# Optimization experiments

Hardware: AMD Instinct MI355X
Metric: run time of the kernel (lower is better)

## Reference

```python
import jax, jax.numpy as jnp
import numpy as np

BATCH = 16384
INPUT_DIM = 1024
OUTPUT_DIM = 256
SCALES = 5  # pywt level = SCALES - 1

# pywt db4 decomposition low-pass filter (ascending index order)
DB4_LO = jnp.array([
    -0.010597401785069032, 0.0328830116668852, 0.030841381835560764,
    -0.18703481171909309, -0.027983769416859854, 0.6308807679298589,
    0.7148465705529157, 0.2303778133088965], dtype=jnp.float32)
# QMF: dec_hi[k] = (-1)^(k+1) * dec_lo[L-1-k]  (matches pywt sign convention)
_SIGNS = jnp.array([-1.0, 1.0, -1.0, 1.0, -1.0, 1.0, -1.0, 1.0], dtype=jnp.float32)
DB4_HI = DB4_LO[::-1] * _SIGNS


def _dwt_step(x, lo, hi):
    """Single-level pywt dwt with 'symmetric' mode along the last axis.
    x: [B, N] -> (cA, cD) each [B, floor((N+L-1)/2)]."""
    L = lo.shape[0]
    left = x[:, L - 2::-1]          # symmetric (half-point) left extension, L-1 samples
    right = x[:, -1:-L:-1]          # symmetric right extension, L-1 samples
    e = jnp.concatenate([left, x, right], axis=-1)[:, 1:]  # drop 1 to align odd-index downsample
    # convolution == correlation with reversed filter; stride-2 valid conv
    kern = jnp.stack([lo[::-1], hi[::-1]])[:, None, :]      # [2, 1, L]
    y = jax.lax.conv_general_dilated(
        e[:, None, :], kern, window_strides=(2,), padding='VALID',
        dimension_numbers=('NCW', 'OIW', 'NCW'))            # [B, 2, out_len]
    return y[:, 0], y[:, 1]


def _wavedec(x, level):
    """pywt.wavedec(x, 'db4', level) -> [cA_level, cD_level, ..., cD_1]."""
    ca = x
    details = []
    for _ in range(level):
        ca, cd = _dwt_step(ca, DB4_LO, DB4_HI)
        details.append(cd)
    return [ca] + details[::-1]


def setup_inputs() -> dict:
    key = jax.random.key(0)
    ks = jax.random.split(key, SCALES + 1)
    inp = {"x": jax.random.normal(ks[0], (BATCH, INPUT_DIM), dtype=jnp.float32)}
    for s in range(SCALES):
        inp[f"basis{s}"] = jax.random.normal(
            ks[s + 1], (INPUT_DIM // 2 ** s, OUTPUT_DIM), dtype=jnp.float32)
    return inp


def reference(x, basis0, basis1, basis2, basis3, basis4):
    bases = [basis0, basis1, basis2, basis3, basis4]
    coeffs = _wavedec(x, SCALES - 1)  # [cA4, cD4, cD3, cD2, cD1]
    out = jnp.zeros((x.shape[0], OUTPUT_DIM), dtype=x.dtype)
    for s in range(SCALES):
        m = min(coeffs[s].shape[-1], bases[s].shape[0])  # static; truncate to common length
        out = out + coeffs[s][:, :m] @ bases[s][:m]
    return out
```

## Files before the change

### kernel.cpp

```cpp
#include <hip/hip_runtime.h>
#include <stdint.h>

#define BATCH   16384
#define INDIM   1024
#define OUTDIM  256

constexpr int KP = 480;

typedef __attribute__((ext_vector_type(8))) short short8;
typedef __attribute__((ext_vector_type(4))) float f32x4;

__device__ __constant__ float LORc[8] = { 0.2303778133088965f,   0.7148465705529157f,
                                          0.6308807679298589f,  -0.027983769416859854f,
                                         -0.18703481171909309f,  0.030841381835560764f,
                                          0.0328830116668852f,  -0.010597401785069032f };
__device__ __constant__ float HIRc[8] = {-0.010597401785069032f, -0.0328830116668852f,
                                          0.030841381835560764f,  0.18703481171909309f,
                                         -0.027983769416859854f, -0.6308807679298589f,
                                          0.7148465705529157f,   -0.2303778133088965f };

__device__ __forceinline__ float symx(const float* __restrict__ in, int N, int t) {
    if (t < 0)  t = -1 - t;
    if (t >= N) t = 2 * N - 1 - t;
    return in[t];
}

__device__ __forceinline__ void dwt_level(const float* __restrict__ in, int N, int M,
                                          float* __restrict__ outA,
                                          float* __restrict__ outD, int nD, int lane) {
    for (int i = lane; i < M; i += 64) {
        const int base = 2 * i - 6;
        float a = 0.f, d = 0.f;
        if (base >= 0 && base + 7 < N) {
            #pragma unroll
            for (int k = 0; k < 8; ++k) {
                const float v = in[base + k];
                a = fmaf(v, LORc[k], a);
                d = fmaf(v, HIRc[k], d);
            }
        } else {
            #pragma unroll
            for (int k = 0; k < 8; ++k) {
                const float v = symx(in, N, base + k);
                a = fmaf(v, LORc[k], a);
                d = fmaf(v, HIRc[k], d);
            }
        }
        outA[i] = a;
        if (i < nD) outD[i] = d;
    }
}

__device__ __forceinline__ ushort f2bf_rne(float f) {
    union { float f; uint32_t u; } v; v.f = f;
    uint32_t r = v.u + 0x7fffu + ((v.u >> 16) & 1u);
    return (ushort)(r >> 16);
}
__device__ __forceinline__ float bf2f(ushort h) {
    union { uint32_t u; float f; } v; v.u = ((uint32_t)h) << 16;
    return v.f;
}

__device__ __forceinline__ void split2(float a0, float a1, uint32_t& hw, uint32_t& lw) {
    const uint32_t u0 = __float_as_uint(a0), u1 = __float_as_uint(a1);
    const uint32_t r0 = u0 + 0x7fffu + ((u0 >> 16) & 1u);
    const uint32_t r1 = u1 + 0x7fffu + ((u1 >> 16) & 1u);
    hw = (r0 >> 16) | (r1 & 0xffff0000u);
    const float l0 = a0 - __uint_as_float(r0 & 0xffff0000u);
    const float l1 = a1 - __uint_as_float(r1 & 0xffff0000u);
    const uint32_t v0 = __float_as_uint(l0), v1 = __float_as_uint(l1);
    const uint32_t s0 = v0 + 0x7fffu + ((v0 >> 16) & 1u);
    const uint32_t s1 = v1 + 0x7fffu + ((v1 >> 16) & 1u);
    lw = (s0 >> 16) | (s1 & 0xffff0000u);
}

extern "C" __global__ __launch_bounds__(256)
void prep1(const float* __restrict__ b0, const float* __restrict__ b1,
           const float* __restrict__ b2, const float* __restrict__ b3,
           const float* __restrict__ b4,
           float* __restrict__ Wc, float* __restrict__ Bp)
{
    __shared__ float buf[4][1544];
    const int tid = threadIdx.x;
    if (blockIdx.x < 256) {
        const int wid  = tid >> 6;
        const int lane = tid & 63;
        const int row  = blockIdx.x * 4 + wid;
        float* bufA = buf[wid];
        float* bufB = bufA + 1024;
        float* crow = Wc + (size_t)row * KP;
        for (int j = lane; j < 1024; j += 64) bufA[j] = (j == row) ? 1.f : 0.f;
        __syncthreads();
        dwt_level(bufA, 1024, 515, bufB, crow + 408, 64, lane);
        __syncthreads();
        dwt_level(bufB, 515, 261, bufA, crow + 280, 128, lane);
        __syncthreads();
        dwt_level(bufA, 261, 134, bufB, crow + 144, 134, lane);
        __syncthreads();
        dwt_level(bufB, 134, 70, crow, crow + 72, 70, lane);
        if (lane < 14) {
            const int padidx[14] = {70,71,142,143,278,279,472,473,474,475,476,477,478,479};
            crow[padidx[lane]] = 0.f;
        }
    } else {
        const int k  = (blockIdx.x - 256) * 4 + (tid >> 6);
        const int n0 = (tid & 63) * 4;
        float4 v = float4{0.f, 0.f, 0.f, 0.f};
        if      (k < 70)              v = *(const float4*)(b0 + (size_t)k * OUTDIM + n0);
        else if (k >= 72  && k < 142) v = *(const float4*)(b1 + (size_t)(k - 72)  * OUTDIM + n0);
        else if (k >= 144 && k < 278) v = *(const float4*)(b2 + (size_t)(k - 144) * OUTDIM + n0);
        else if (k >= 280 && k < 408) v = *(const float4*)(b3 + (size_t)(k - 280) * OUTDIM + n0);
        else if (k >= 408 && k < 472) v = *(const float4*)(b4 + (size_t)(k - 408) * OUTDIM + n0);
        *(float4*)(Bp + (size_t)k * OUTDIM + n0) = v;
    }
}

extern "C" __global__ __launch_bounds__(256)
void prep2(const float* __restrict__ Wc, const float* __restrict__ Bp,
           ushort* __restrict__ Bpk)
{
    __shared__ float wc[8][KP];
    const int tid = threadIdx.x;
    const int k0  = blockIdx.x * 8;
    const int r   = tid >> 5;
    for (int k = (tid & 31); k < KP; k += 32)
        wc[r][k] = Wc[(size_t)(k0 + r) * KP + k];
    __syncthreads();

    float acc[8] = {0,0,0,0,0,0,0,0};
    for (int k = 0; k < KP; ++k) {
        const float b = Bp[(size_t)k * OUTDIM + tid];
        #pragma unroll
        for (int j = 0; j < 8; ++j) acc[j] = fmaf(wc[j][k], b, acc[j]);
    }

    const int chunk = blockIdx.x >> 2, kg = blockIdx.x & 3;
    const int nf = tid >> 4, ln = tid & 15;
    const int lane = kg * 16 + ln;
    ushort h[8], l[8];
    #pragma unroll
    for (int j = 0; j < 8; ++j) {
        h[j] = f2bf_rne(acc[j]);
        l[j] = f2bf_rne(acc[j] - bf2f(h[j]));
    }
    const size_t base = ((size_t)(chunk * 16 + nf) * 2) * 512 + (size_t)lane * 8;
    uint4 hv = { (uint32_t)h[0] | ((uint32_t)h[1] << 16), (uint32_t)h[2] | ((uint32_t)h[3] << 16),
                 (uint32_t)h[4] | ((uint32_t)h[5] << 16), (uint32_t)h[6] | ((uint32_t)h[7] << 16) };
    uint4 lv = { (uint32_t)l[0] | ((uint32_t)l[1] << 16), (uint32_t)l[2] | ((uint32_t)l[3] << 16),
                 (uint32_t)l[4] | ((uint32_t)l[5] << 16), (uint32_t)l[6] | ((uint32_t)l[7] << 16) };
    *(uint4*)(Bpk + base)       = hv;
    *(uint4*)(Bpk + base + 512) = lv;
}

extern "C" __global__ __launch_bounds__(512, 4)
void wkan_mfma(const float* __restrict__ x, const ushort* __restrict__ Bpk,
               float* __restrict__ out)
{
    __shared__ ushort Bb[2][8][2][64][8];
    __shared__ ushort Ah[2][2][2][2][64][8];

    const int tid  = threadIdx.x;
    const int lane = tid & 63;
    const int wid  = tid >> 6;
    const int wm   = wid >> 2;
    const int wn   = wid & 3;
    const int row0 = blockIdx.x * 64;
    const int nf0  = blockIdx.y * 8;

    const int srow  = tid >> 3;
    const int sk0   = (tid & 7) << 2;
    const int slane = (sk0 >> 3) * 16 + (srow & 15);
    const int sj0   = sk0 & 7;
    const int swm   = srow >> 5, smf = (srow >> 4) & 1;

    const float*  agp = x + (size_t)(row0 + srow) * INDIM + sk0;
    const ushort* bgp = Bpk + (size_t)nf0 * 1024 + (size_t)tid * 8;

    f32x4 acc[2][2];
    #pragma unroll
    for (int m = 0; m < 2; ++m)
        #pragma unroll
        for (int f = 0; f < 2; ++f) acc[m][f] = f32x4{0.f, 0.f, 0.f, 0.f};

    float4 av; uint4 bv0, bv1;

    av  = *(const float4*)(agp);
    bv0 = *(const uint4*)(bgp);
    bv1 = *(const uint4*)(bgp + 4096);
    {
        uint32_t hw0, lw0, hw1, lw1;
        split2(av.x, av.y, hw0, lw0);
        split2(av.z, av.w, hw1, lw1);
        *(uint2*)&Ah[0][swm][smf][0][slane][sj0] = uint2{hw0, hw1};
        *(uint2*)&Ah[0][swm][smf][1][slane][sj0] = uint2{lw0, lw1};
        ushort* bd = &Bb[0][0][0][0][0] + (size_t)tid * 8;
        *(uint4*)bd          = bv0;
        *(uint4*)(bd + 4096) = bv1;
    }
    av  = *(const float4*)(agp + 32);
    bv0 = *(const uint4*)(bgp + 16384);
    bv1 = *(const uint4*)(bgp + 16384 + 4096);
    __syncthreads();

    for (int c = 0; c < 32; ++c) {
        const int cur = c & 1, nx = cur ^ 1;

        if (c < 31) {
            uint32_t hw0, lw0, hw1, lw1;
            split2(av.x, av.y, hw0, lw0);
            split2(av.z, av.w, hw1, lw1);
            *(uint2*)&Ah[nx][swm][smf][0][slane][sj0] = uint2{hw0, hw1};
            *(uint2*)&Ah[nx][swm][smf][1][slane][sj0] = uint2{lw0, lw1};
            ushort* bd = &Bb[nx][0][0][0][0] + (size_t)tid * 8;
            *(uint4*)bd          = bv0;
            *(uint4*)(bd + 4096) = bv1;
        }
        if (c < 30) {
            av = *(const float4*)(agp + (size_t)(c + 2) * 32);
            const ushort* bs = bgp + (size_t)(c + 2) * 16384;
            bv0 = *(const uint4*)bs;
            bv1 = *(const uint4*)(bs + 4096);
        }

        short8 afr[2][2], bfr[2][2];
        #pragma unroll
        for (int m = 0; m < 2; ++m)
            #pragma unroll
            for (int h = 0; h < 2; ++h)
                afr[m][h] = *(const short8*)&Ah[cur][wm][m][h][lane][0];
        #pragma unroll
        for (int f = 0; f < 2; ++f)
            #pragma unroll
            for (int h = 0; h < 2; ++h)
                bfr[f][h] = *(const short8*)&Bb[cur][wn * 2 + f][h][lane][0];

        #pragma unroll
        for (int m = 0; m < 2; ++m)
            #pragma unroll
            for (int f = 0; f < 2; ++f) {
                acc[m][f] = __builtin_amdgcn_mfma_f32_16x16x32_bf16(afr[m][0], bfr[f][0], acc[m][f], 0, 0, 0);
                acc[m][f] = __builtin_amdgcn_mfma_f32_16x16x32_bf16(afr[m][0], bfr[f][1], acc[m][f], 0, 0, 0);
                acc[m][f] = __builtin_amdgcn_mfma_f32_16x16x32_bf16(afr[m][1], bfr[f][0], acc[m][f], 0, 0, 0);
            }
        __syncthreads();
    }

    #pragma unroll
    for (int m = 0; m < 2; ++m)
        #pragma unroll
        for (int f = 0; f < 2; ++f) {
            const int col  = nf0 * 16 + wn * 32 + f * 16 + (lane & 15);
            const int rowb = row0 + wm * 32 + m * 16 + (lane >> 4) * 4;
            #pragma unroll
            for (int r = 0; r < 4; ++r)
                out[(size_t)(rowb + r) * OUTDIM + col] = acc[m][f][r];
        }
}

constexpr int F_ROWS = 32;
constexpr int F_KP   = 472;

__device__ __forceinline__ void dwt_level_f(const float* __restrict__ in, int N, int M,
                                            float* __restrict__ outA,
                                            float* __restrict__ outD, int nD, int ht) {
    for (int i = ht; i < M; i += 128) {
        const int base = 2 * i - 6;
        float a = 0.f, d = 0.f;
        #pragma unroll
        for (int k = 0; k < 8; ++k) {
            const float v = symx(in, N, base + k);
            a = fmaf(v, LORc[k], a);
            d = fmaf(v, HIRc[k], d);
        }
        outA[i] = a;
        if (i < nD) outD[i] = d;
    }
}

extern "C" __global__ __launch_bounds__(256, 2)
void wkan_fused(const float* __restrict__ x,
                const float* __restrict__ b0, const float* __restrict__ b1,
                const float* __restrict__ b2, const float* __restrict__ b3,
                const float* __restrict__ b4,
                float* __restrict__ out)
{
    extern __shared__ float smem[];
    float* coef = smem;
    float* wbuf = smem + F_ROWS * F_KP;

    const int tid  = threadIdx.x;
    const int row0 = blockIdx.x * F_ROWS;

    for (int i = tid; i < F_ROWS * F_KP / 4; i += 256)
        ((float4*)coef)[i] = float4{0.f, 0.f, 0.f, 0.f};
    __syncthreads();

    const int slot = tid >> 7;
    const int ht   = tid & 127;
    float* bufA = wbuf + slot * 1544;
    float* bufB = bufA + 1024;

    for (int it = 0; it < F_ROWS / 2; ++it) {
        const int r = it * 2 + slot;
        float* crow = coef + r * F_KP;
        const float* xrow = x + (size_t)(row0 + r) * INDIM;
        ((float4*)bufA)[ht]       = ((const float4*)xrow)[ht];
        ((float4*)bufA)[ht + 128] = ((const float4*)xrow)[ht + 128];
        __syncthreads();
        dwt_level_f(bufA, 1024, 515, bufB, crow + 408, 64, ht);
        __syncthreads();
        dwt_level_f(bufB, 515, 261, bufA, crow + 280, 128, ht);
        __syncthreads();
        dwt_level_f(bufA, 261, 134, bufB, crow + 144, 134, ht);
        __syncthreads();
        dwt_level_f(bufB, 134, 70, crow, crow + 72, 70, ht);
        __syncthreads();
    }

    const int rg = tid >> 5;
    const int cg = tid & 31;
    float acc[4][8];
    #pragma unroll
    for (int r = 0; r < 4; ++r)
        #pragma unroll
        for (int c = 0; c < 8; ++c) acc[r][c] = 0.f;

    const float* Bs[5]  = { b0, b1, b2, b3, b4 };
    const int    off[5] = { 0, 72, 144, 280, 408 };
    const int    l4[5]  = { 72, 72, 136, 128, 64 };

    for (int s = 0; s < 5; ++s) {
        const float* __restrict__ B = Bs[s];
        const int o = off[s], L = l4[s];
        for (int k = 0; k < L; k += 4) {
            float4 bb[4][2];
            #pragma unroll
            for (int kk = 0; kk < 4; ++kk) {
                const float* bp = B + (size_t)(k + kk) * OUTDIM + cg * 8;
                bb[kk][0] = *(const float4*)(bp);
                bb[kk][1] = *(const float4*)(bp + 4);
            }
            #pragma unroll
            for (int rr = 0; rr < 4; ++rr) {
                const float4 c4 = *(const float4*)(coef + (rg * 4 + rr) * F_KP + o + k);
                const float cv[4] = { c4.x, c4.y, c4.z, c4.w };
                #pragma unroll
                for (int kk = 0; kk < 4; ++kk) {
                    acc[rr][0] = fmaf(cv[kk], bb[kk][0].x, acc[rr][0]);
                    acc[rr][1] = fmaf(cv[kk], bb[kk][0].y, acc[rr][1]);
                    acc[rr][2] = fmaf(cv[kk], bb[kk][0].z, acc[rr][2]);
                    acc[rr][3] = fmaf(cv[kk], bb[kk][0].w, acc[rr][3]);
                    acc[rr][4] = fmaf(cv[kk], bb[kk][1].x, acc[rr][4]);
                    acc[rr][5] = fmaf(cv[kk], bb[kk][1].y, acc[rr][5]);
                    acc[rr][6] = fmaf(cv[kk], bb[kk][1].z, acc[rr][6]);
                    acc[rr][7] = fmaf(cv[kk], bb[kk][1].w, acc[rr][7]);
                }
            }
        }
    }

    #pragma unroll
    for (int rr = 0; rr < 4; ++rr) {
        float* op = out + (size_t)(row0 + rg * 4 + rr) * OUTDIM + cg * 8;
        *(float4*)(op)     = float4{ acc[rr][0], acc[rr][1], acc[rr][2], acc[rr][3] };
        *(float4*)(op + 4) = float4{ acc[rr][4], acc[rr][5], acc[rr][6], acc[rr][7] };
    }
}

extern "C" void kernel_launch(void* const* d_in, const int* in_sizes, int n_in,
                              void* d_out, int out_size, void* d_ws, size_t ws_size,
                              hipStream_t stream) {
    const float* x  = (const float*)d_in[0];
    const float* b0 = (const float*)d_in[1];
    const float* b1 = (const float*)d_in[2];
    const float* b2 = (const float*)d_in[3];
    const float* b3 = (const float*)d_in[4];
    const float* b4 = (const float*)d_in[5];
    float* out = (float*)d_out;

    const size_t nWc  = (size_t)1024 * KP;
    const size_t nBp  = (size_t)KP * OUTDIM;
    const size_t nBpk = (size_t)1024 * OUTDIM * 2;
    const size_t need = (nWc + nBp) * 4 + nBpk * 2;

    if (ws_size >= need) {
        float*  Wc  = (float*)d_ws;
        float*  Bp  = Wc + nWc;
        ushort* Bpk = (ushort*)(Bp + nBp);

        hipLaunchKernelGGL(prep1, dim3(376), dim3(256), 0, stream,
                           b0, b1, b2, b3, b4, Wc, Bp);
        hipLaunchKernelGGL(prep2, dim3(128), dim3(256), 0, stream, Wc, Bp, Bpk);
        hipLaunchKernelGGL(wkan_mfma, dim3(BATCH / 64, 2), dim3(512), 0, stream,
                           x, Bpk, out);
    } else {
        const size_t shmem = (size_t)(F_ROWS * F_KP + 2 * 1544) * sizeof(float);
        hipLaunchKernelGGL(wkan_fused, dim3(BATCH / F_ROWS), dim3(256), shmem, stream,
                           x, b0, b1, b2, b3, b4, out);
    }
}
```

Measured before the change: 160.9 us.

## Widen MFMA tile to full output width and deepen x prefetch

The main GEMM kernel now has each block compute all 256 output columns instead of splitting N across two blocks. This removes the duplicate loading and bf16 splitting of x rows, at the cost of twice the B staging per block and dynamic LDS of 80KB. The x loads are prefetched four chunks ahead through a small register ring. The A hi part now uses truncation instead of round-to-nearest before the residual split. __syncthreads is replaced by an explicit lgkmcnt wait plus s_barrier, and the occupancy hint in launch bounds is dropped.

```diff
diff --git a/kernel.cpp b/kernel.cpp
--- a/kernel.cpp
+++ b/kernel.cpp
@@ -61,13 +61,11 @@
     return v.f;
 }
 
-__device__ __forceinline__ void split2(float a0, float a1, uint32_t& hw, uint32_t& lw) {
+__device__ __forceinline__ void splitc(float a0, float a1, uint32_t& hw, uint32_t& lw) {
     const uint32_t u0 = __float_as_uint(a0), u1 = __float_as_uint(a1);
-    const uint32_t r0 = u0 + 0x7fffu + ((u0 >> 16) & 1u);
-    const uint32_t r1 = u1 + 0x7fffu + ((u1 >> 16) & 1u);
-    hw = (r0 >> 16) | (r1 & 0xffff0000u);
-    const float l0 = a0 - __uint_as_float(r0 & 0xffff0000u);
-    const float l1 = a1 - __uint_as_float(r1 & 0xffff0000u);
+    hw = (u0 >> 16) | (u1 & 0xffff0000u);
+    const float l0 = a0 - __uint_as_float(u0 & 0xffff0000u);
+    const float l1 = a1 - __uint_as_float(u1 & 0xffff0000u);
     const uint32_t v0 = __float_as_uint(l0), v1 = __float_as_uint(l1);
     const uint32_t s0 = v0 + 0x7fffu + ((v0 >> 16) & 1u);
     const uint32_t s1 = v1 + 0x7fffu + ((v1 >> 16) & 1u);
@@ -152,12 +150,13 @@
     *(uint4*)(Bpk + base + 512) = lv;
 }
 
-extern "C" __global__ __launch_bounds__(512, 4)
+extern "C" __global__ __launch_bounds__(512)
 void wkan_mfma(const float* __restrict__ x, const ushort* __restrict__ Bpk,
                float* __restrict__ out)
 {
-    __shared__ ushort Bb[2][8][2][64][8];
-    __shared__ ushort Ah[2][2][2][2][64][8];
+    extern __shared__ __align__(16) ushort sm[];
+    ushort* Bb0 = sm;
+    ushort* Ah0 = sm + 32768;
 
     const int tid  = threadIdx.x;
     const int lane = tid & 63;
@@ -165,91 +164,113 @@
     const int wm   = wid >> 2;
     const int wn   = wid & 3;
     const int row0 = blockIdx.x * 64;
-    const int nf0  = blockIdx.y * 8;
-
-    const int srow  = tid >> 3;
-    const int sk0   = (tid & 7) << 2;
-    const int slane = (sk0 >> 3) * 16 + (srow & 15);
-    const int sj0   = sk0 & 7;
-    const int swm   = srow >> 5, smf = (srow >> 4) & 1;
-
+
+    const int srow = tid >> 3;
+    const int sk0  = (tid & 7) << 2;
+    const int smf  = srow >> 4;
+    const int slan = ((sk0 >> 3) << 4) | (srow & 15);
+    const int sj0  = sk0 & 7;
+    const int awoff = ((smf * 2 + 0) * 64 + slan) * 8 + sj0;
     const float*  agp = x + (size_t)(row0 + srow) * INDIM + sk0;
-    const ushort* bgp = Bpk + (size_t)nf0 * 1024 + (size_t)tid * 8;
-
-    f32x4 acc[2][2];
+    const ushort* bgp = Bpk + (size_t)tid * 8;
+
+    f32x4 acc[2][4];
     #pragma unroll
     for (int m = 0; m < 2; ++m)
         #pragma unroll
-        for (int f = 0; f < 2; ++f) acc[m][f] = f32x4{0.f, 0.f, 0.f, 0.f};
-
-    float4 av; uint4 bv0, bv1;
-
-    av  = *(const float4*)(agp);
+        for (int f = 0; f < 4; ++f) acc[m][f] = f32x4{0.f, 0.f, 0.f, 0.f};
+
+    float4 av[4];
+    uint4  bv0, bv1, bv2, bv3;
+
+    av[0] = *(const float4*)agp;
     bv0 = *(const uint4*)(bgp);
     bv1 = *(const uint4*)(bgp + 4096);
+    bv2 = *(const uint4*)(bgp + 8192);
+    bv3 = *(const uint4*)(bgp + 12288);
+    av[1] = *(const float4*)(agp + 32);
+    av[2] = *(const float4*)(agp + 64);
+    av[3] = *(const float4*)(agp + 96);
     {
         uint32_t hw0, lw0, hw1, lw1;
-        split2(av.x, av.y, hw0, lw0);
-        split2(av.z, av.w, hw1, lw1);
-        *(uint2*)&Ah[0][swm][smf][0][slane][sj0] = uint2{hw0, hw1};
-        *(uint2*)&Ah[0][swm][smf][1][slane][sj0] = uint2{lw0, lw1};
-        ushort* bd = &Bb[0][0][0][0][0] + (size_t)tid * 8;
-        *(uint4*)bd          = bv0;
-        *(uint4*)(bd + 4096) = bv1;
-    }
-    av  = *(const float4*)(agp + 32);
-    bv0 = *(const uint4*)(bgp + 16384);
-    bv1 = *(const uint4*)(bgp + 16384 + 4096);
-    __syncthreads();
-
+        splitc(av[0].x, av[0].y, hw0, lw0);
+        splitc(av[0].z, av[0].w, hw1, lw1);
+        *(uint2*)(Ah0 + awoff)       = uint2{hw0, hw1};
+        *(uint2*)(Ah0 + awoff + 512) = uint2{lw0, lw1};
+        ushort* bd = Bb0 + tid * 8;
+        *(uint4*)(bd)         = bv0;
+        *(uint4*)(bd + 4096)  = bv1;
+        *(uint4*)(bd + 8192)  = bv2;
+        *(uint4*)(bd + 12288) = bv3;
+    }
+    {
+        const ushort* bs = bgp + 16384;
+        bv0 = *(const uint4*)(bs);
+        bv1 = *(const uint4*)(bs + 4096);
+        bv2 = *(const uint4*)(bs + 8192);
+        bv3 = *(const uint4*)(bs + 12288);
+    }
+    asm volatile("s_waitcnt lgkmcnt(0)\n\ts_barrier" ::: "memory");
+
+    #pragma unroll 4
     for (int c = 0; c < 32; ++c) {
-        const int cur = c & 1, nx = cur ^ 1;
+        const int cur = c & 1;
+        ushort* Bbc = Bb0 + cur * 16384;
+        ushort* Ahc = Ah0 + cur * 4096;
+        ushort* Bbn = Bb0 + (cur ^ 1) * 16384;
+        ushort* Ahn = Ah0 + (cur ^ 1) * 4096;
 
         if (c < 31) {
+            const float4 a = av[(c + 1) & 3];
             uint32_t hw0, lw0, hw1, lw1;
-            split2(av.x, av.y, hw0, lw0);
-            split2(av.z, av.w, hw1, lw1);
-            *(uint2*)&Ah[nx][swm][smf][0][slane][sj0] = uint2{hw0, hw1};
-            *(uint2*)&Ah[nx][swm][smf][1][slane][sj0] = uint2{lw0, lw1};
-            ushort* bd = &Bb[nx][0][0][0][0] + (size_t)tid * 8;
-            *(uint4*)bd          = bv0;
-            *(uint4*)(bd + 4096) = bv1;
+            splitc(a.x, a.y, hw0, lw0);
+            splitc(a.z, a.w, hw1, lw1);
+            *(uint2*)(Ahn + awoff)       = uint2{hw0, hw1};
+            *(uint2*)(Ahn + awoff + 512) = uint2{lw0, lw1};
+            ushort* bd = Bbn + tid * 8;
+            *(uint4*)(bd)         = bv0;
+            *(uint4*)(bd + 4096)  = bv1;
+            *(uint4*)(bd + 8192)  = bv2;
+            *(uint4*)(bd + 12288) = bv3;
         }
         if (c < 30) {
-            av = *(const float4*)(agp + (size_t)(c + 2) * 32);
             const ushort* bs = bgp + (size_t)(c + 2) * 16384;
-            bv0 = *(const uint4*)bs;
+            bv0 = *(const uint4*)(bs);
             bv1 = *(const uint4*)(bs + 4096);
-        }
-
-        short8 afr[2][2], bfr[2][2];
+            bv2 = *(const uint4*)(bs + 8192);
+            bv3 = *(const uint4*)(bs + 12288);
+        }
+        if (c < 28) av[c & 3] = *(const float4*)(agp + (size_t)(c + 4) * 32);
+
+        short8 afr[2][2], bfr[4][2];
         #pragma unroll
         for (int m = 0; m < 2; ++m)
             #pragma unroll
             for (int h = 0; h < 2; ++h)
-                afr[m][h] = *(const short8*)&Ah[cur][wm][m][h][lane][0];
-        #pragma unroll
-        for (int f = 0; f < 2; ++f)
+                afr[m][h] = *(const short8*)(Ahc + (((wm * 2 + m) * 2 + h) * 64 + lane) * 8);
+        #pragma unroll
+        for (int f = 0; f < 4; ++f)
             #pragma unroll
             for (int h = 0; h < 2; ++h)
-                bfr[f][h] = *(const short8*)&Bb[cur][wn * 2 + f][h][lane][0];
+                bfr[f][h] = *(const short8*)(Bbc + (((wn * 4 + f) * 2 + h) * 64 + lane) * 8);
 
         #pragma unroll
         for (int m = 0; m < 2; ++m)
             #pragma unroll
-            for (int f = 0; f < 2; ++f) {
+            for (int f = 0; f < 4; ++f) {
                 acc[m][f] = __builtin_amdgcn_mfma_f32_16x16x32_bf16(afr[m][0], bfr[f][0], acc[m][f], 0, 0, 0);
                 acc[m][f] = __builtin_amdgcn_mfma_f32_16x16x32_bf16(afr[m][0], bfr[f][1], acc[m][f], 0, 0, 0);
                 acc[m][f] = __builtin_amdgcn_mfma_f32_16x16x32_bf16(afr[m][1], bfr[f][0], acc[m][f], 0, 0, 0);
             }
-        __syncthreads();
+
+        asm volatile("s_waitcnt lgkmcnt(0)\n\ts_barrier" ::: "memory");
     }
 
     #pragma unroll
     for (int m = 0; m < 2; ++m)
         #pragma unroll
-        for (int f = 0; f < 2; ++f) {
-            const int col  = nf0 * 16 + wn * 32 + f * 16 + (lane & 15);
+        for (int f = 0; f < 4; ++f) {
+            const int col  = wn * 64 + f * 16 + (lane & 15);
             const int rowb = row0 + wm * 32 + m * 16 + (lane >> 4) * 4;
             #pragma unroll
             for (int r = 0; r < 4; ++r)
@@ -388,10 +409,13 @@
         float*  Bp  = Wc + nWc;
         ushort* Bpk = (ushort*)(Bp + nBp);
 
+        hipFuncSetAttribute(reinterpret_cast<const void*>(wkan_mfma),
+                            hipFuncAttributeMaxDynamicSharedMemorySize, 81920);
+
         hipLaunchKernelGGL(prep1, dim3(376), dim3(256), 0, stream,
                            b0, b1, b2, b3, b4, Wc, Bp);
         hipLaunchKernelGGL(prep2, dim3(128), dim3(256), 0, stream, Wc, Bp, Bpk);
-        hipLaunchKernelGGL(wkan_mfma, dim3(BATCH / 64, 2), dim3(512), 0, stream,
+        hipLaunchKernelGGL(wkan_mfma, dim3(BATCH / 64), dim3(512), 81920, stream,
                            x, Bpk, out);
     } else {
         const size_t shmem = (size_t)(F_ROWS * F_KP + 2 * 1544) * sizeof(float);
```

Measured after the change: 159.0 us. No clear change (-1.2%).

## Load MFMA operands directly from global into registers, drop LDS staging

Applied to the files above, without the earlier changes.

The main GEMM kernel no longer stages A and B through shared memory with barriers. Each wave now loads its bf16-split B fragments and fp32 x rows straight into registers, double-buffered across iterations, and covers 32 rows by 64 columns per wave. The A hi-part split becomes truncation instead of round-to-nearest, which saves ALU work. prep2 is reorganised with a transposed shared-memory layout and a 2D grid for more parallelism. In exchange, x rows are re-read by the 4 column-blocks, and global loads are less coalesced than the old LDS staging.

```diff
diff --git a/kernel.cpp b/kernel.cpp
--- a/kernel.cpp
+++ b/kernel.cpp
@@ -61,13 +61,11 @@
     return v.f;
 }
 
-__device__ __forceinline__ void split2(float a0, float a1, uint32_t& hw, uint32_t& lw) {
+__device__ __forceinline__ void splitc(float a0, float a1, uint32_t& hw, uint32_t& lw) {
     const uint32_t u0 = __float_as_uint(a0), u1 = __float_as_uint(a1);
-    const uint32_t r0 = u0 + 0x7fffu + ((u0 >> 16) & 1u);
-    const uint32_t r1 = u1 + 0x7fffu + ((u1 >> 16) & 1u);
-    hw = (r0 >> 16) | (r1 & 0xffff0000u);
-    const float l0 = a0 - __uint_as_float(r0 & 0xffff0000u);
-    const float l1 = a1 - __uint_as_float(r1 & 0xffff0000u);
+    hw = (u0 >> 16) | (u1 & 0xffff0000u);
+    const float l0 = a0 - __uint_as_float(u0 & 0xffff0000u);
+    const float l1 = a1 - __uint_as_float(u1 & 0xffff0000u);
     const uint32_t v0 = __float_as_uint(l0), v1 = __float_as_uint(l1);
     const uint32_t s0 = v0 + 0x7fffu + ((v0 >> 16) & 1u);
     const uint32_t s1 = v1 + 0x7fffu + ((v1 >> 16) & 1u);
@@ -119,31 +117,45 @@
 void prep2(const float* __restrict__ Wc, const float* __restrict__ Bp,
            ushort* __restrict__ Bpk)
 {
-    __shared__ float wc[8][KP];
+    __shared__ float wcT[KP][32];
     const int tid = threadIdx.x;
-    const int k0  = blockIdx.x * 8;
-    const int r   = tid >> 5;
-    for (int k = (tid & 31); k < KP; k += 32)
-        wc[r][k] = Wc[(size_t)(k0 + r) * KP + k];
+    const int c   = blockIdx.x;
+    const int nq  = blockIdx.y;
+    const int n   = nq * 64 + (tid & 63);
+    const int ms  = tid >> 6;
+
+    {
+        const int mm = tid >> 3, t8 = tid & 7;
+        const float* src = Wc + (size_t)(c * 32 + mm) * KP;
+        for (int k = t8 * 4; k < KP; k += 32) {
+            const float4 v = *(const float4*)(src + k);
+            wcT[k + 0][mm] = v.x; wcT[k + 1][mm] = v.y;
+            wcT[k + 2][mm] = v.z; wcT[k + 3][mm] = v.w;
+        }
+    }
     __syncthreads();
 
     float acc[8] = {0,0,0,0,0,0,0,0};
+    #pragma unroll 4
     for (int k = 0; k < KP; ++k) {
-        const float b = Bp[(size_t)k * OUTDIM + tid];
-        #pragma unroll
-        for (int j = 0; j < 8; ++j) acc[j] = fmaf(wc[j][k], b, acc[j]);
-    }
-
-    const int chunk = blockIdx.x >> 2, kg = blockIdx.x & 3;
-    const int nf = tid >> 4, ln = tid & 15;
-    const int lane = kg * 16 + ln;
+        const float bpv = Bp[(size_t)k * OUTDIM + n];
+        const float4 w0 = *(const float4*)&wcT[k][ms * 8];
+        const float4 w1 = *(const float4*)&wcT[k][ms * 8 + 4];
+        acc[0] = fmaf(w0.x, bpv, acc[0]); acc[1] = fmaf(w0.y, bpv, acc[1]);
+        acc[2] = fmaf(w0.z, bpv, acc[2]); acc[3] = fmaf(w0.w, bpv, acc[3]);
+        acc[4] = fmaf(w1.x, bpv, acc[4]); acc[5] = fmaf(w1.y, bpv, acc[5]);
+        acc[6] = fmaf(w1.z, bpv, acc[6]); acc[7] = fmaf(w1.w, bpv, acc[7]);
+    }
+
     ushort h[8], l[8];
     #pragma unroll
     for (int j = 0; j < 8; ++j) {
         h[j] = f2bf_rne(acc[j]);
         l[j] = f2bf_rne(acc[j] - bf2f(h[j]));
     }
-    const size_t base = ((size_t)(chunk * 16 + nf) * 2) * 512 + (size_t)lane * 8;
+    const int nf   = n >> 4;
+    const int lane = ms * 16 + (n & 15);
+    const size_t base = (size_t)c * 16384 + (size_t)(nf * 2) * 512 + (size_t)lane * 8;
     uint4 hv = { (uint32_t)h[0] | ((uint32_t)h[1] << 16), (uint32_t)h[2] | ((uint32_t)h[3] << 16),
                  (uint32_t)h[4] | ((uint32_t)h[5] << 16), (uint32_t)h[6] | ((uint32_t)h[7] << 16) };
     uint4 lv = { (uint32_t)l[0] | ((uint32_t)l[1] << 16), (uint32_t)l[2] | ((uint32_t)l[3] << 16),
@@ -152,105 +164,92 @@
     *(uint4*)(Bpk + base + 512) = lv;
 }
 
-extern "C" __global__ __launch_bounds__(512, 4)
-void wkan_mfma(const float* __restrict__ x, const ushort* __restrict__ Bpk,
-               float* __restrict__ out)
+extern "C" __global__ __launch_bounds__(256)
+void wkan_direct(const float* __restrict__ x, const ushort* __restrict__ Bpk,
+                 float* __restrict__ out)
 {
-    __shared__ ushort Bb[2][8][2][64][8];
-    __shared__ ushort Ah[2][2][2][2][64][8];
-
     const int tid  = threadIdx.x;
     const int lane = tid & 63;
-    const int wid  = tid >> 6;
-    const int wm   = wid >> 2;
-    const int wn   = wid & 3;
-    const int row0 = blockIdx.x * 64;
-    const int nf0  = blockIdx.y * 8;
-
-    const int srow  = tid >> 3;
-    const int sk0   = (tid & 7) << 2;
-    const int slane = (sk0 >> 3) * 16 + (srow & 15);
-    const int sj0   = sk0 & 7;
-    const int swm   = srow >> 5, smf = (srow >> 4) & 1;
-
-    const float*  agp = x + (size_t)(row0 + srow) * INDIM + sk0;
-    const ushort* bgp = Bpk + (size_t)nf0 * 1024 + (size_t)tid * 8;
-
-    f32x4 acc[2][2];
+    const int w    = tid >> 6;
+    const int row0 = blockIdx.x * 128 + w * 32;
+    const int nf0  = blockIdx.y * 4;
+
+    const int r15 = lane & 15;
+    const int kg  = lane >> 4;
+
+    const float*  a0 = x + (size_t)(row0 + r15) * INDIM + kg * 8;
+    const float*  a1 = a0 + (size_t)16 * INDIM;
+    const ushort* bp = Bpk + (size_t)nf0 * 1024 + (size_t)lane * 8;
+
+    f32x4 acc[2][4];
     #pragma unroll
     for (int m = 0; m < 2; ++m)
         #pragma unroll
-        for (int f = 0; f < 2; ++f) acc[m][f] = f32x4{0.f, 0.f, 0.f, 0.f};
-
-    float4 av; uint4 bv0, bv1;
-
-    av  = *(const float4*)(agp);
-    bv0 = *(const uint4*)(bgp);
-    bv1 = *(const uint4*)(bgp + 4096);
-    {
-        uint32_t hw0, lw0, hw1, lw1;
-        split2(av.x, av.y, hw0, lw0);
-        split2(av.z, av.w, hw1, lw1);
-        *(uint2*)&Ah[0][swm][smf][0][slane][sj0] = uint2{hw0, hw1};
-        *(uint2*)&Ah[0][swm][smf][1][slane][sj0] = uint2{lw0, lw1};
-        ushort* bd = &Bb[0][0][0][0][0] + (size_t)tid * 8;
-        *(uint4*)bd          = bv0;
-        *(uint4*)(bd + 4096) = bv1;
-    }
-    av  = *(const float4*)(agp + 32);
-    bv0 = *(const uint4*)(bgp + 16384);
-    bv1 = *(const uint4*)(bgp + 16384 + 4096);
-    __syncthreads();
-
+        for (int f = 0; f < 4; ++f) acc[m][f] = f32x4{0.f, 0.f, 0.f, 0.f};
+
+    float4 ar[2][2][2];
+    uint4  br[2][4][2];
+
+    #pragma unroll
+    for (int f = 0; f < 4; ++f) {
+        br[0][f][0] = *(const uint4*)(bp + f * 1024);
+        br[0][f][1] = *(const uint4*)(bp + f * 1024 + 512);
+    }
+    ar[0][0][0] = *(const float4*)(a0);
+    ar[0][0][1] = *(const float4*)(a0 + 4);
+    ar[0][1][0] = *(const float4*)(a1);
+    ar[0][1][1] = *(const float4*)(a1 + 4);
+
+    #pragma unroll 2
     for (int c = 0; c < 32; ++c) {
-        const int cur = c & 1, nx = cur ^ 1;
+        const int p = c & 1, q = p ^ 1;
 
         if (c < 31) {
-            uint32_t hw0, lw0, hw1, lw1;
-            split2(av.x, av.y, hw0, lw0);
-            split2(av.z, av.w, hw1, lw1);
-            *(uint2*)&Ah[nx][swm][smf][0][slane][sj0] = uint2{hw0, hw1};
-            *(uint2*)&Ah[nx][swm][smf][1][slane][sj0] = uint2{lw0, lw1};
-            ushort* bd = &Bb[nx][0][0][0][0] + (size_t)tid * 8;
-            *(uint4*)bd          = bv0;
-            *(uint4*)(bd + 4096) = bv1;
-        }
-        if (c < 30) {
-            av = *(const float4*)(agp + (size_t)(c + 2) * 32);
-            const ushort* bs = bgp + (size_t)(c + 2) * 16384;
-            bv0 = *(const uint4*)bs;
-            bv1 = *(const uint4*)(bs + 4096);
-        }
-
-        short8 afr[2][2], bfr[2][2];
+            const ushort* bn = bp + (size_t)(c + 1) * 16384;
+            #pragma unroll
+            for (int f = 0; f < 4; ++f) {
+                br[q][f][0] = *(const uint4*)(bn + f * 1024);
+                br[q][f][1] = *(const uint4*)(bn + f * 1024 + 512);
+            }
+            const float* an0 = a0 + (size_t)(c + 1) * 32;
+            const float* an1 = a1 + (size_t)(c + 1) * 32;
+            ar[q][0][0] = *(const float4*)(an0);
+            ar[q][0][1] = *(const float4*)(an0 + 4);
+            ar[q][1][0] = *(const float4*)(an1);
+            ar[q][1][1] = *(const float4*)(an1 + 4);
+        }
+
+        short8 afr[2][2];
+        #pragma unroll
+        for (int m = 0; m < 2; ++m) {
+            union { uint32_t u[4]; short8 s; } uh, ul;
+            splitc(ar[p][m][0].x, ar[p][m][0].y, uh.u[0], ul.u[0]);
+            splitc(ar[p][m][0].z, ar[p][m][0].w, uh.u[1], ul.u[1]);
+            splitc(ar[p][m][1].x, ar[p][m][1].y, uh.u[2], ul.u[2]);
+            splitc(ar[p][m][1].z, ar[p][m][1].w, uh.u[3], ul.u[3]);
+            afr[m][0] = uh.s;
+            afr[m][1] = ul.s;
+        }
+
         #pragma unroll
         for (int m = 0; m < 2; ++m)
             #pragma unroll
-            for (int h = 0; h < 2; ++h)
-                afr[m][h] = *(const short8*)&Ah[cur][wm][m][h][lane][0];
-        #pragma unroll
-        for (int f = 0; f < 2; ++f)
-            #pragma unroll
-            for (int h = 0; h < 2; ++h)
-                bfr[f][h] = *(const short8*)&Bb[cur][wn * 2 + f][h][lane][0];
-
-        #pragma unroll
-        for (int m = 0; m < 2; ++m)
-            #pragma unroll
-            for (int f = 0; f < 2; ++f) {
-                acc[m][f] = __builtin_amdgcn_mfma_f32_16x16x32_bf16(afr[m][0], bfr[f][0], acc[m][f], 0, 0, 0);
-                acc[m][f] = __builtin_amdgcn_mfma_f32_16x16x32_bf16(afr[m][0], bfr[f][1], acc[m][f], 0, 0, 0);
-                acc[m][f] = __builtin_amdgcn_mfma_f32_16x16x32_bf16(afr[m][1], bfr[f][0], acc[m][f], 0, 0, 0);
-            }
-        __syncthreads();
+            for (int f = 0; f < 4; ++f) {
+                union { uint4 u; short8 s; } b0c, b1c;
+                b0c.u = br[p][f][0];
+                b1c.u = br[p][f][1];
+                acc[m][f] = __builtin_amdgcn_mfma_f32_16x16x32_bf16(afr[m][0], b0c.s, acc[m][f], 0, 0, 0);
+                acc[m][f] = __builtin_amdgcn_mfma_f32_16x16x32_bf16(afr[m][0], b1c.s, acc[m][f], 0, 0, 0);
+                acc[m][f] = __builtin_amdgcn_mfma_f32_16x16x32_bf16(afr[m][1], b0c.s, acc[m][f], 0, 0, 0);
+            }
     }
 
     #pragma unroll
     for (int m = 0; m < 2; ++m)
         #pragma unroll
-        for (int f = 0; f < 2; ++f) {
-            const int col  = nf0 * 16 + wn * 32 + f * 16 + (lane & 15);
-            const int rowb = row0 + wm * 32 + m * 16 + (lane >> 4) * 4;
+        for (int f = 0; f < 4; ++f) {
+            const int col  = nf0 * 16 + f * 16 + r15;
+            const int rowb = row0 + m * 16 + kg * 4;
             #pragma unroll
             for (int r = 0; r < 4; ++r)
                 out[(size_t)(rowb + r) * OUTDIM + col] = acc[m][f][r];
@@ -336,9 +335,9 @@
             float4 bb[4][2];
             #pragma unroll
             for (int kk = 0; kk < 4; ++kk) {
-                const float* bp = B + (size_t)(k + kk) * OUTDIM + cg * 8;
-                bb[kk][0] = *(const float4*)(bp);
-                bb[kk][1] = *(const float4*)(bp + 4);
+                const float* bpp = B + (size_t)(k + kk) * OUTDIM + cg * 8;
+                bb[kk][0] = *(const float4*)(bpp);
+                bb[kk][1] = *(const float4*)(bpp + 4);
             }
             #pragma unroll
             for (int rr = 0; rr < 4; ++rr) {
@@ -390,8 +389,8 @@
 
         hipLaunchKernelGGL(prep1, dim3(376), dim3(256), 0, stream,
                            b0, b1, b2, b3, b4, Wc, Bp);
-        hipLaunchKernelGGL(prep2, dim3(128), dim3(256), 0, stream, Wc, Bp, Bpk);
-        hipLaunchKernelGGL(wkan_mfma, dim3(BATCH / 64, 2), dim3(512), 0, stream,
+        hipLaunchKernelGGL(prep2, dim3(32, 4), dim3(256), 0, stream, Wc, Bp, Bpk);
+        hipLaunchKernelGGL(wkan_direct, dim3(BATCH / 128, 4), dim3(256), 0, stream,
                            x, Bpk, out);
     } else {
         const size_t shmem = (size_t)(F_ROWS * F_KP + 2 * 1544) * sizeof(float);
```

After: 509.4 us. +216.6%, slower.
